# Performance work log

Measured on AMD Instinct MI355X. Metric: run time of the kernel, lower is better.

Reference implementation:

```python
import jax, jax.numpy as jnp
import numpy as np

VOCAB, DIM = 100000, 512
BATCH, SEQ = 4096, 200
HID, OUT = 256, 20


def setup_inputs() -> dict:
    key = jax.random.key(0)
    k_emb, k_x, k_len, k_w1, k_b1, k_w2, k_b2 = jax.random.split(key, 7)
    emb_table = jax.random.normal(k_emb, (VOCAB, DIM), dtype=jnp.float32) * 0.1
    x = jax.random.randint(k_x, (BATCH, SEQ), 0, VOCAB, dtype=jnp.int64)
    # lengths in [1, SEQ] to avoid division by zero, matching real padded batches
    lengths = jax.random.randint(k_len, (BATCH,), 1, SEQ + 1, dtype=jnp.int64)
    bows = jnp.zeros((BATCH,), dtype=jnp.float32)  # unused by the model's forward
    # Linear(2*DIM, 256) and Linear(256, OUT); stored transposed for x @ W
    W1 = jax.random.normal(k_w1, (2 * DIM, HID), dtype=jnp.float32) * (1.0 / np.sqrt(2 * DIM))
    b1 = jax.random.normal(k_b1, (HID,), dtype=jnp.float32) * 0.01
    W2 = jax.random.normal(k_w2, (HID, OUT), dtype=jnp.float32) * (1.0 / np.sqrt(HID))
    b2 = jax.random.normal(k_b2, (OUT,), dtype=jnp.float32) * 0.01
    return {"emb_table": emb_table, "W1": W1, "b1": b1, "W2": W2, "b2": b2,
            "x": x, "lengths": lengths, "bows": bows}


def reference(emb_table, W1, b1, W2, b2, x, lengths, bows):
    # Gather: [B, S, D]
    emb = emb_table[x]
    # Faithful to original: sum over the FULL sequence (padding included),
    # divided by the true length; max also over the full sequence.
    rep_mean = jnp.sum(emb, axis=1) / lengths.astype(emb.dtype)[:, None]  # [B, D]
    rep_max = jnp.max(emb, axis=1)                                        # [B, D]
    rep = jnp.concatenate([rep_mean, rep_max], axis=1)                    # [B, 2D]
    h = jax.nn.relu(rep @ W1 + b1)                                        # [B, 256]
    logits = h @ W2 + b2                                                  # [B, OUT]
    return logits
```

## Files before the change

### kernel.cpp

```cpp
#include <hip/hip_runtime.h>
#include <hip/hip_bf16.h>

#define VOCAB 100000
#define DIM   512
#define BATCH 4096
#define SEQ   200
#define HID   256
#define OUTN  20

typedef __attribute__((ext_vector_type(8))) short short8;
typedef __attribute__((ext_vector_type(4))) float floatx4;

static __device__ __forceinline__ unsigned short f2bf(float f) {
    __hip_bfloat16 b = __float2bfloat16(f);
    return *(unsigned short*)&b;
}
static __device__ __forceinline__ float bf2f(unsigned short u) {
    unsigned int v = (unsigned int)u << 16;
    return *(float*)&v;
}

__global__ __launch_bounds__(256) void k_cvt(
    const float* __restrict__ src, unsigned short* __restrict__ dst)
{
    const int n8 = VOCAB * DIM / 8;
    int i = blockIdx.x * 256 + threadIdx.x;
    const int stride = gridDim.x * 256;
    const floatx4* s4 = (const floatx4*)src;
    short8* d8 = (short8*)dst;
    for (; i < n8; i += stride) {
        const floatx4 a = __builtin_nontemporal_load(&s4[2 * i]);
        const floatx4 b = __builtin_nontemporal_load(&s4[2 * i + 1]);
        short8 o;
        o[0] = (short)f2bf(a[0]); o[1] = (short)f2bf(a[1]);
        o[2] = (short)f2bf(a[2]); o[3] = (short)f2bf(a[3]);
        o[4] = (short)f2bf(b[0]); o[5] = (short)f2bf(b[1]);
        o[6] = (short)f2bf(b[2]); o[7] = (short)f2bf(b[3]);
        d8[i] = o;
    }
}

__global__ __launch_bounds__(256) void k_reduce_bf(
    const unsigned short* __restrict__ embb, const int* __restrict__ x,
    const int* __restrict__ lengths, unsigned short* __restrict__ repb)
{
    const int b = blockIdx.x;
    const int t = threadIdx.x;
    const int w = t >> 6;
    const int lane = t & 63;

    __shared__ int sidx[SEQ];
    for (int i = t; i < SEQ; i += 256) sidx[i] = x[b * SEQ + i];
    __syncthreads();

    float s[8] = {0.f, 0.f, 0.f, 0.f, 0.f, 0.f, 0.f, 0.f};
    float m[8] = {-1e30f, -1e30f, -1e30f, -1e30f, -1e30f, -1e30f, -1e30f, -1e30f};

    const unsigned short* base = embb + lane * 8;
    const int i0 = w * (SEQ / 4);

#pragma unroll 5
    for (int i = i0; i < i0 + SEQ / 4; ++i) {
        const short8 v = *(const short8*)(base + (size_t)sidx[i] * DIM);
#pragma unroll
        for (int j = 0; j < 8; ++j) {
            const float f = bf2f((unsigned short)v[j]);
            s[j] += f;
            m[j] = fmaxf(m[j], f);
        }
    }

    __shared__ float red[4][2][DIM];
#pragma unroll
    for (int j = 0; j < 8; ++j) {
        red[w][0][lane * 8 + j] = s[j];
        red[w][1][lane * 8 + j] = m[j];
    }
    __syncthreads();

    const float inv = 1.0f / (float)lengths[b];
    const int c0 = t * 2;
    unsigned int mu = 0, xu = 0;
#pragma unroll
    for (int j = 0; j < 2; ++j) {
        const float sv = red[0][0][c0 + j] + red[1][0][c0 + j]
                       + red[2][0][c0 + j] + red[3][0][c0 + j];
        const float mv = fmaxf(fmaxf(red[0][1][c0 + j], red[1][1][c0 + j]),
                               fmaxf(red[2][1][c0 + j], red[3][1][c0 + j]));
        mu |= (unsigned int)f2bf(sv * inv) << (16 * j);
        xu |= (unsigned int)f2bf(mv)       << (16 * j);
    }
    unsigned short* row = repb + (size_t)b * (2 * DIM);
    *(unsigned int*)(row + c0)       = mu;
    *(unsigned int*)(row + DIM + c0) = xu;
}

__global__ __launch_bounds__(128) void k_reduce(
    const float* __restrict__ emb, const int* __restrict__ x,
    const int* __restrict__ lengths, unsigned short* __restrict__ repb)
{
    const int b = blockIdx.x;
    const int t = threadIdx.x;

    __shared__ int sidx[SEQ];
    for (int i = t; i < SEQ; i += 128) sidx[i] = x[b * SEQ + i];
    __syncthreads();

    const float4* embv = (const float4*)emb;
    float4 s = make_float4(0.f, 0.f, 0.f, 0.f);
    float4 m = make_float4(-1e30f, -1e30f, -1e30f, -1e30f);

#pragma unroll 4
    for (int i = 0; i < SEQ; ++i) {
        const float4 v = embv[(size_t)sidx[i] * (DIM / 4) + t];
        s.x += v.x; s.y += v.y; s.z += v.z; s.w += v.w;
        m.x = fmaxf(m.x, v.x); m.y = fmaxf(m.y, v.y);
        m.z = fmaxf(m.z, v.z); m.w = fmaxf(m.w, v.w);
    }

    const float inv = 1.0f / (float)lengths[b];
    unsigned long long mu =
          (unsigned long long)f2bf(s.x * inv)
        | ((unsigned long long)f2bf(s.y * inv) << 16)
        | ((unsigned long long)f2bf(s.z * inv) << 32)
        | ((unsigned long long)f2bf(s.w * inv) << 48);
    unsigned long long xu =
          (unsigned long long)f2bf(m.x)
        | ((unsigned long long)f2bf(m.y) << 16)
        | ((unsigned long long)f2bf(m.z) << 32)
        | ((unsigned long long)f2bf(m.w) << 48);

    unsigned short* row = repb + (size_t)b * (2 * DIM);
    *(unsigned long long*)(row + 4 * t)       = mu;
    *(unsigned long long*)(row + DIM + 4 * t) = xu;
}

__global__ __launch_bounds__(256) void k_w1t(
    const float* __restrict__ W1, unsigned short* __restrict__ W1T)
{
    __shared__ unsigned short s[64][65];
    const int n0 = blockIdx.x * 64;
    const int k0 = blockIdx.y * 64;
    const int t = threadIdx.x;

#pragma unroll
    for (int i = 0; i < 4; ++i) {
        const int kk = (t >> 4) + i * 16;
        const int cc = (t & 15) * 4;
        const float4 v = *(const float4*)&W1[(size_t)(k0 + kk) * HID + n0 + cc];
        s[cc + 0][kk] = f2bf(v.x);
        s[cc + 1][kk] = f2bf(v.y);
        s[cc + 2][kk] = f2bf(v.z);
        s[cc + 3][kk] = f2bf(v.w);
    }
    __syncthreads();

#pragma unroll
    for (int i = 0; i < 4; ++i) {
        const int nn = (t >> 4) + i * 16;
        const int kq = (t & 15) * 4;
        unsigned long long u =
              (unsigned long long)s[nn][kq + 0]
            | ((unsigned long long)s[nn][kq + 1] << 16)
            | ((unsigned long long)s[nn][kq + 2] << 32)
            | ((unsigned long long)s[nn][kq + 3] << 48);
        *(unsigned long long*)&W1T[(size_t)(n0 + nn) * (2 * DIM) + k0 + kq] = u;
    }
}

#define APAD 40

__global__ __launch_bounds__(256) void k_gemm1(
    const unsigned short* __restrict__ repb,
    const unsigned short* __restrict__ w1t,
    const float* __restrict__ bias, float* __restrict__ h)
{
    const int K = 2 * DIM;
    const int rowBase = blockIdx.y * 64;
    const int colBase = blockIdx.x * 64;
    const int tid  = threadIdx.x;
    const int lane = tid & 63;
    const int wv   = tid >> 6;
    const int wm   = wv & 1;
    const int wn   = wv >> 1;

    __shared__ unsigned short sA[64][APAD];
    __shared__ unsigned short sB[64][APAD];

    const int r  = tid >> 2;
    const int kq = tid & 3;

    const unsigned short* gA = repb + (size_t)(rowBase + r) * K + kq * 8;
    const unsigned short* gB = w1t  + (size_t)(colBase + r) * K + kq * 8;

    floatx4 acc[2][2] = {{{0.f,0.f,0.f,0.f},{0.f,0.f,0.f,0.f}},
                         {{0.f,0.f,0.f,0.f},{0.f,0.f,0.f,0.f}}};

    short8 pa = *(const short8*)gA;
    short8 pb = *(const short8*)gB;

    const int lm = lane & 15;
    const int lq = lane >> 4;
    for (int k0 = 0; k0 < K; k0 += 32) {
        __syncthreads();
        *(short8*)&sA[r][kq * 8] = pa;
        *(short8*)&sB[r][kq * 8] = pb;
        __syncthreads();

        if (k0 + 32 < K) {
            pa = *(const short8*)(gA + k0 + 32);
            pb = *(const short8*)(gB + k0 + 32);
        }

        const short8 a0 = *(const short8*)&sA[wm * 32 + lm][lq * 8];
        const short8 a1 = *(const short8*)&sA[wm * 32 + 16 + lm][lq * 8];
        const short8 b0 = *(const short8*)&sB[wn * 32 + lm][lq * 8];
        const short8 b1 = *(const short8*)&sB[wn * 32 + 16 + lm][lq * 8];

        acc[0][0] = __builtin_amdgcn_mfma_f32_16x16x32_bf16(a0, b0, acc[0][0], 0, 0, 0);
        acc[0][1] = __builtin_amdgcn_mfma_f32_16x16x32_bf16(a0, b1, acc[0][1], 0, 0, 0);
        acc[1][0] = __builtin_amdgcn_mfma_f32_16x16x32_bf16(a1, b0, acc[1][0], 0, 0, 0);
        acc[1][1] = __builtin_amdgcn_mfma_f32_16x16x32_bf16(a1, b1, acc[1][1], 0, 0, 0);
    }

#pragma unroll
    for (int nt = 0; nt < 2; ++nt) {
        const int col = colBase + wn * 32 + nt * 16 + lm;
        const float bb = bias[col];
#pragma unroll
        for (int mt = 0; mt < 2; ++mt) {
#pragma unroll
            for (int rg = 0; rg < 4; ++rg) {
                const int row = rowBase + wm * 32 + mt * 16 + lq * 4 + rg;
                h[(size_t)row * HID + col] = fmaxf(acc[mt][nt][rg] + bb, 0.f);
            }
        }
    }
}

#define R3 32
#define HP4 260

__global__ __launch_bounds__(256) void k_gemm2(
    const float* __restrict__ H, const float* __restrict__ W2,
    const float* __restrict__ b2, float* __restrict__ outp)
{
    __shared__ float sh[R3][HP4];
    __shared__ float swt[OUTN][HP4];
    __shared__ float sb[OUTN];

    const int t = threadIdx.x;
    const int rowBase = blockIdx.x * R3;

    const float4* H4 = (const float4*)H;
    for (int i = t; i < R3 * (HID / 4); i += 256) {
        const int r  = i >> 6;
        const int c4 = i & 63;
        *(float4*)&sh[r][c4 * 4] = H4[(size_t)(rowBase + r) * (HID / 4) + c4];
    }
    {
        const int k = t;
#pragma unroll
        for (int c = 0; c < OUTN; ++c) swt[c][k] = W2[k * OUTN + c];
    }
    if (t < OUTN) sb[t] = b2[t];
    __syncthreads();

    const int r  = t & 31;
    const int cs = t >> 5;
    float a0 = sb[cs], a1 = sb[cs + 8], a2 = (cs + 16 < OUTN) ? sb[cs + 16] : 0.f;
    float acc0 = 0.f, acc1 = 0.f, acc2 = 0.f;

#pragma unroll 8
    for (int k = 0; k < HID; k += 4) {
        const float4 a = *(const float4*)&sh[r][k];
        const float4 w0 = *(const float4*)&swt[cs][k];
        const float4 w1 = *(const float4*)&swt[cs + 8][k];
        acc0 += a.x * w0.x + a.y * w0.y + a.z * w0.z + a.w * w0.w;
        acc1 += a.x * w1.x + a.y * w1.y + a.z * w1.z + a.w * w1.w;
        if (cs + 16 < OUTN) {
            const float4 w2 = *(const float4*)&swt[cs + 16][k];
            acc2 += a.x * w2.x + a.y * w2.y + a.z * w2.z + a.w * w2.w;
        }
    }

    float* orow = outp + (size_t)(rowBase + r) * OUTN;
    orow[cs]     = acc0 + a0;
    orow[cs + 8] = acc1 + a1;
    if (cs + 16 < OUTN) orow[cs + 16] = acc2 + a2;
}

extern "C" void kernel_launch(void* const* d_in, const int* in_sizes, int n_in,
                              void* d_out, int out_size, void* d_ws, size_t ws_size,
                              hipStream_t stream)
{
    const float* emb     = (const float*)d_in[0];
    const float* W1      = (const float*)d_in[1];
    const float* b1      = (const float*)d_in[2];
    const float* W2      = (const float*)d_in[3];
    const float* b2      = (const float*)d_in[4];
    const int*   x       = (const int*)d_in[5];
    const int*   lengths = (const int*)d_in[6];

    float* out = (float*)d_out;

    const size_t embbN = (size_t)VOCAB * DIM;
    const size_t repbN = (size_t)BATCH * 2 * DIM;
    const size_t w1tN  = (size_t)HID * 2 * DIM;
    const size_t hN    = (size_t)BATCH * HID;
    const size_t needFast = (embbN + repbN + w1tN) * 2 + hN * 4 + 256;

    if (ws_size >= needFast) {
        unsigned short* embb = (unsigned short*)d_ws;
        unsigned short* repb = embb + embbN;
        unsigned short* w1t  = repb + repbN;
        float* h = (float*)(w1t + w1tN);

        k_cvt<<<2048, 256, 0, stream>>>(emb, embb);
        k_w1t<<<dim3(HID / 64, (2 * DIM) / 64), 256, 0, stream>>>(W1, w1t);
        k_reduce_bf<<<BATCH, 256, 0, stream>>>(embb, x, lengths, repb);
        k_gemm1<<<dim3(HID / 64, BATCH / 64), 256, 0, stream>>>(repb, w1t, b1, h);
        k_gemm2<<<BATCH / R3, 256, 0, stream>>>(h, W2, b2, out);
    } else {
        unsigned short* repb = (unsigned short*)d_ws;
        unsigned short* w1t  = repb + repbN;
        float* h = (float*)(w1t + w1tN);

        k_w1t<<<dim3(HID / 64, (2 * DIM) / 64), 256, 0, stream>>>(W1, w1t);
        k_reduce<<<BATCH, 128, 0, stream>>>(emb, x, lengths, repb);
        k_gemm1<<<dim3(HID / 64, BATCH / 64), 256, 0, stream>>>(repb, w1t, b1, h);
        k_gemm2<<<BATCH / R3, 256, 0, stream>>>(h, W2, b2, out);
    }
}
```

Measured before the change: 421.4 us.

## Fuse GEMM1 and GEMM2 into one kernel and widen reduce blocks

The two MLP layers now run in one kernel. Each block computes a 32-row tile of the hidden layer with bf16 MFMA, stores it ReLU'd in shared memory and then applies the second linear layer, so the fp32 hidden matrix never goes to global memory and one launch is removed. The gather-reduce kernel moves to 512 threads (8 waves, each covering 25 sequence positions), precomputes byte offsets and uses vectorized shared stores. The fused GEMM grid has only 128 blocks, which may leave much of the GPU idle compared with the earlier tiled GEMM1.

```diff
diff --git a/kernel.cpp b/kernel.cpp
--- a/kernel.cpp
+++ b/kernel.cpp
@@ -40,7 +40,7 @@
     }
 }
 
-__global__ __launch_bounds__(256) void k_reduce_bf(
+__global__ __launch_bounds__(512) void k_reduce_bf(
     const unsigned short* __restrict__ embb, const int* __restrict__ x,
     const int* __restrict__ lengths, unsigned short* __restrict__ repb)
 {
@@ -50,18 +50,18 @@
     const int lane = t & 63;
 
     __shared__ int sidx[SEQ];
-    for (int i = t; i < SEQ; i += 256) sidx[i] = x[b * SEQ + i];
+    if (t < SEQ) sidx[t] = x[b * SEQ + t] * (DIM * 2);
     __syncthreads();
 
     float s[8] = {0.f, 0.f, 0.f, 0.f, 0.f, 0.f, 0.f, 0.f};
     float m[8] = {-1e30f, -1e30f, -1e30f, -1e30f, -1e30f, -1e30f, -1e30f, -1e30f};
 
-    const unsigned short* base = embb + lane * 8;
-    const int i0 = w * (SEQ / 4);
+    const char* base = (const char*)embb + lane * 16;
+    const int i0 = w * (SEQ / 8);
 
 #pragma unroll 5
-    for (int i = i0; i < i0 + SEQ / 4; ++i) {
-        const short8 v = *(const short8*)(base + (size_t)sidx[i] * DIM);
+    for (int i = i0; i < i0 + SEQ / 8; ++i) {
+        const short8 v = *(const short8*)(base + sidx[i]);
 #pragma unroll
         for (int j = 0; j < 8; ++j) {
             const float f = bf2f((unsigned short)v[j]);
@@ -70,29 +70,25 @@
         }
     }
 
-    __shared__ float red[4][2][DIM];
-#pragma unroll
-    for (int j = 0; j < 8; ++j) {
-        red[w][0][lane * 8 + j] = s[j];
-        red[w][1][lane * 8 + j] = m[j];
-    }
+    __shared__ float red[8][2][DIM];
+    *(float4*)&red[w][0][lane * 8]     = make_float4(s[0], s[1], s[2], s[3]);
+    *(float4*)&red[w][0][lane * 8 + 4] = make_float4(s[4], s[5], s[6], s[7]);
+    *(float4*)&red[w][1][lane * 8]     = make_float4(m[0], m[1], m[2], m[3]);
+    *(float4*)&red[w][1][lane * 8 + 4] = make_float4(m[4], m[5], m[6], m[7]);
     __syncthreads();
 
     const float inv = 1.0f / (float)lengths[b];
-    const int c0 = t * 2;
-    unsigned int mu = 0, xu = 0;
-#pragma unroll
-    for (int j = 0; j < 2; ++j) {
-        const float sv = red[0][0][c0 + j] + red[1][0][c0 + j]
-                       + red[2][0][c0 + j] + red[3][0][c0 + j];
-        const float mv = fmaxf(fmaxf(red[0][1][c0 + j], red[1][1][c0 + j]),
-                               fmaxf(red[2][1][c0 + j], red[3][1][c0 + j]));
-        mu |= (unsigned int)f2bf(sv * inv) << (16 * j);
-        xu |= (unsigned int)f2bf(mv)       << (16 * j);
+    const int c = t;
+    float sv = red[0][0][c];
+    float mv = red[0][1][c];
+#pragma unroll
+    for (int ww = 1; ww < 8; ++ww) {
+        sv += red[ww][0][c];
+        mv = fmaxf(mv, red[ww][1][c]);
     }
     unsigned short* row = repb + (size_t)b * (2 * DIM);
-    *(unsigned int*)(row + c0)       = mu;
-    *(unsigned int*)(row + DIM + c0) = xu;
+    row[c]       = f2bf(sv * inv);
+    row[DIM + c] = f2bf(mv);
 }
 
 __global__ __launch_bounds__(128) void k_reduce(
@@ -168,6 +164,122 @@
     }
 }
 
+#define BM3 32
+#define BK3 64
+#define SPAD 72
+#define HP4 260
+
+__global__ __launch_bounds__(256) void k_fused(
+    const unsigned short* __restrict__ repb,
+    const unsigned short* __restrict__ w1t,
+    const float* __restrict__ b1,
+    const float* __restrict__ W2,
+    const float* __restrict__ b2,
+    float* __restrict__ outp)
+{
+    __shared__ __align__(16) char smem[54080];
+    unsigned short (*sA)[SPAD] = (unsigned short(*)[SPAD])smem;
+    unsigned short (*sB)[SPAD] = (unsigned short(*)[SPAD])(smem + BM3 * SPAD * 2);
+    float (*sh)[HP4]  = (float(*)[HP4])smem;
+    float (*swt)[HP4] = (float(*)[HP4])(smem + BM3 * HP4 * 4);
+    __shared__ float sb2[OUTN];
+
+    const int K = 2 * DIM;
+    const int rowBase = blockIdx.x * BM3;
+    const int t = threadIdx.x;
+    const int lane = t & 63;
+    const int wv = t >> 6;
+    const int lm = lane & 15;
+    const int lq = lane >> 4;
+
+    const int ar = t >> 3;
+    const int ac = t & 7;
+    const unsigned short* gA = repb + (size_t)(rowBase + ar) * K + ac * 8;
+    const unsigned short* gB = w1t + (size_t)t * K;
+
+    floatx4 acc[2][4];
+#pragma unroll
+    for (int i = 0; i < 2; ++i)
+#pragma unroll
+        for (int j = 0; j < 4; ++j)
+            acc[i][j] = (floatx4){0.f, 0.f, 0.f, 0.f};
+
+    short8 pa = *(const short8*)gA;
+    short8 pb[8];
+#pragma unroll
+    for (int cth = 0; cth < 8; ++cth) pb[cth] = *(const short8*)(gB + cth * 8);
+
+    for (int k0 = 0; k0 < K; k0 += BK3) {
+        __syncthreads();
+        *(short8*)&sA[ar][ac * 8] = pa;
+#pragma unroll
+        for (int cth = 0; cth < 8; ++cth) *(short8*)&sB[t][cth * 8] = pb[cth];
+        __syncthreads();
+
+        if (k0 + BK3 < K) {
+            pa = *(const short8*)(gA + k0 + BK3);
+#pragma unroll
+            for (int cth = 0; cth < 8; ++cth)
+                pb[cth] = *(const short8*)(gB + k0 + BK3 + cth * 8);
+        }
+
+#pragma unroll
+        for (int ks = 0; ks < 2; ++ks) {
+            const short8 a0 = *(const short8*)&sA[lm][ks * 32 + lq * 8];
+            const short8 a1 = *(const short8*)&sA[16 + lm][ks * 32 + lq * 8];
+#pragma unroll
+            for (int nt = 0; nt < 4; ++nt) {
+                const short8 bfr = *(const short8*)&sB[wv * 64 + nt * 16 + lm][ks * 32 + lq * 8];
+                acc[0][nt] = __builtin_amdgcn_mfma_f32_16x16x32_bf16(a0, bfr, acc[0][nt], 0, 0, 0);
+                acc[1][nt] = __builtin_amdgcn_mfma_f32_16x16x32_bf16(a1, bfr, acc[1][nt], 0, 0, 0);
+            }
+        }
+    }
+
+    __syncthreads();
+
+#pragma unroll
+    for (int nt = 0; nt < 4; ++nt) {
+        const int col = wv * 64 + nt * 16 + lm;
+        const float bb = b1[col];
+#pragma unroll
+        for (int mt = 0; mt < 2; ++mt) {
+#pragma unroll
+            for (int rg = 0; rg < 4; ++rg) {
+                const int row = mt * 16 + lq * 4 + rg;
+                sh[row][col] = fmaxf(acc[mt][nt][rg] + bb, 0.f);
+            }
+        }
+    }
+    {
+        const int k = t;
+#pragma unroll
+        for (int cc = 0; cc < OUTN; ++cc) swt[cc][k] = W2[k * OUTN + cc];
+    }
+    if (t < OUTN) sb2[t] = b2[t];
+    __syncthreads();
+
+    const int r  = t >> 3;
+    const int cs = t & 7;
+    float acc0 = 0.f, acc1 = 0.f, acc2 = 0.f;
+#pragma unroll 8
+    for (int k = 0; k < HID; k += 4) {
+        const float4 a  = *(const float4*)&sh[r][k];
+        const float4 w0 = *(const float4*)&swt[cs][k];
+        const float4 w1v = *(const float4*)&swt[cs + 8][k];
+        acc0 += a.x * w0.x + a.y * w0.y + a.z * w0.z + a.w * w0.w;
+        acc1 += a.x * w1v.x + a.y * w1v.y + a.z * w1v.z + a.w * w1v.w;
+        if (cs + 16 < OUTN) {
+            const float4 w2v = *(const float4*)&swt[cs + 16][k];
+            acc2 += a.x * w2v.x + a.y * w2v.y + a.z * w2v.z + a.w * w2v.w;
+        }
+    }
+    float* orow = outp + (size_t)(rowBase + r) * OUTN;
+    orow[cs]     = acc0 + sb2[cs];
+    orow[cs + 8] = acc1 + sb2[cs + 8];
+    if (cs + 16 < OUTN) orow[cs + 16] = acc2 + sb2[cs + 16];
+}
+
 #define APAD 40
 
 __global__ __launch_bounds__(256) void k_gemm1(
@@ -239,7 +351,6 @@
 }
 
 #define R3 32
-#define HP4 260
 
 __global__ __launch_bounds__(256) void k_gemm2(
     const float* __restrict__ H, const float* __restrict__ W2,
@@ -308,19 +419,17 @@
     const size_t repbN = (size_t)BATCH * 2 * DIM;
     const size_t w1tN  = (size_t)HID * 2 * DIM;
     const size_t hN    = (size_t)BATCH * HID;
-    const size_t needFast = (embbN + repbN + w1tN) * 2 + hN * 4 + 256;
+    const size_t needFast = (embbN + repbN + w1tN) * 2 + 256;
 
     if (ws_size >= needFast) {
         unsigned short* embb = (unsigned short*)d_ws;
         unsigned short* repb = embb + embbN;
         unsigned short* w1t  = repb + repbN;
-        float* h = (float*)(w1t + w1tN);
 
         k_cvt<<<2048, 256, 0, stream>>>(emb, embb);
         k_w1t<<<dim3(HID / 64, (2 * DIM) / 64), 256, 0, stream>>>(W1, w1t);
-        k_reduce_bf<<<BATCH, 256, 0, stream>>>(embb, x, lengths, repb);
-        k_gemm1<<<dim3(HID / 64, BATCH / 64), 256, 0, stream>>>(repb, w1t, b1, h);
-        k_gemm2<<<BATCH / R3, 256, 0, stream>>>(h, W2, b2, out);
+        k_reduce_bf<<<BATCH, 512, 0, stream>>>(embb, x, lengths, repb);
+        k_fused<<<BATCH / BM3, 256, 0, stream>>>(repb, w1t, b1, W2, b2, out);
     } else {
         unsigned short* repb = (unsigned short*)d_ws;
         unsigned short* w1t  = repb + repbN;
```

Result: no change. 429.4 us (+1.9%).
